# Kernel tuning notes

Measured on AMD Instinct MI355X. Metric: run time of the kernel, lower is better.

## Reference

```python
import jax, jax.numpy as jnp
import numpy as np

B, C = 8192, 4096

def _to_complex(r):
    # (..., 2) real/imag stack -> complex
    return jax.lax.complex(r[..., 0], r[..., 1])

def _to_real(z):
    return jnp.stack([jnp.real(z), jnp.imag(z)], axis=-1)

def setup_inputs() -> dict:
    key = jax.random.key(0)
    kx, ka, kd = jax.random.split(key, 3)
    x = jax.random.normal(kx, (B, C, 2), dtype=jnp.float32)
    # A, D ~ Normal(1.0, 0.01) per reset_parameters
    A = 1.0 + 0.01 * jax.random.normal(ka, (1, C, 2), dtype=jnp.float32)
    D = 1.0 + 0.01 * jax.random.normal(kd, (1, C, 2), dtype=jnp.float32)
    return {"x": x, "A": A, "D": D}

def reference(x, A, D):
    # Elementwise scale (real and imag parts scaled independently, NOT complex mul)
    xs = A * x                                   # (B, C, 2)
    # torch.fft(x, 1): complex FFT over the signal dim (channels, dim 1)
    f = jnp.fft.fft(_to_complex(xs), axis=1)     # (B, C) complex64
    fs = D * _to_real(f)                         # elementwise scale in real/imag repr
    # torch.ifft is normalized by 1/N, same as jnp.fft.ifft
    out = jnp.fft.ifft(_to_complex(fs), axis=1)  # (B, C) complex64
    return _to_real(out)                         # (B, C, 2)
```

## Files before the change

kernel.cpp:

```cpp
#include <hip/hip_runtime.h>

#define FFT_N   4096
#define THREADS 256

__device__ __forceinline__ float2 cmul(float2 a, float2 b) {
    return make_float2(a.x*b.x - a.y*b.y, a.x*b.y + a.y*b.x);
}
__device__ __forceinline__ float2 cadd(float2 a, float2 b){ return make_float2(a.x+b.x, a.y+b.y); }
__device__ __forceinline__ float2 csub(float2 a, float2 b){ return make_float2(a.x-b.x, a.y-b.y); }

template<int S>
__device__ __forceinline__ float2 muli(float2 z) {
    return (S < 0) ? make_float2(z.y, -z.x) : make_float2(-z.y, z.x);
}

template<int S>
__device__ __forceinline__ void dft4(float2 a0, float2 a1, float2 a2, float2 a3,
                                     float2& y0, float2& y1, float2& y2, float2& y3) {
    float2 e0 = cadd(a0, a2), e1 = cadd(a1, a3);
    float2 o0 = csub(a0, a2), o1 = muli<S>(csub(a1, a3));
    y0 = cadd(e0, e1); y2 = csub(e0, e1);
    y1 = cadd(o0, o1); y3 = csub(o0, o1);
}

template<int S>
__device__ __forceinline__ void dft16(float2* a) {
    const float C1 = 0.92387953251128674f;
    const float S1 = 0.38268343236508978f;
    const float R2 = 0.70710678118654752f;
    const float sg = (S < 0) ? -1.0f : 1.0f;
    const float2 w1 = make_float2( C1,  sg*S1);
    const float2 w2 = make_float2( R2,  sg*R2);
    const float2 w3 = make_float2( S1,  sg*C1);
    const float2 w6 = make_float2(-R2,  sg*R2);
    const float2 w9 = make_float2(-C1, -sg*S1);
    float2 t[16];
    dft4<S>(a[0], a[4], a[8],  a[12], t[0],  t[1],  t[2],  t[3]);
    dft4<S>(a[1], a[5], a[9],  a[13], t[4],  t[5],  t[6],  t[7]);
    dft4<S>(a[2], a[6], a[10], a[14], t[8],  t[9],  t[10], t[11]);
    dft4<S>(a[3], a[7], a[11], a[15], t[12], t[13], t[14], t[15]);
    t[5]  = cmul(t[5],  w1);  t[6]  = cmul(t[6],  w2);  t[7]  = cmul(t[7],  w3);
    t[9]  = cmul(t[9],  w2);  t[10] = muli<S>(t[10]);   t[11] = cmul(t[11], w6);
    t[13] = cmul(t[13], w3);  t[14] = cmul(t[14], w6);  t[15] = cmul(t[15], w9);
    dft4<S>(t[0], t[4], t[8],  t[12], a[0], a[4], a[8],  a[12]);
    dft4<S>(t[1], t[5], t[9],  t[13], a[1], a[5], a[9],  a[13]);
    dft4<S>(t[2], t[6], t[10], t[14], a[2], a[6], a[10], a[14]);
    dft4<S>(t[3], t[7], t[11], t[15], a[3], a[7], a[11], a[15]);
}

template<int S>
__device__ __forceinline__ void twiddle_apply(float2* R, int p, float invM) {
    float ang = 6.283185307179586f * (float)p * invM;
    if (S < 0) ang = -ang;
    float s, c;
    __sincosf(ang, &s, &c);
    float2 w[16];
    w[1] = make_float2(c, s);
    w[2] = cmul(w[1], w[1]);
    w[3] = cmul(w[2], w[1]);
    w[4] = cmul(w[2], w[2]);
    #pragma unroll
    for (int k = 5; k < 16; ++k) w[k] = cmul(w[k-4], w[4]);
    #pragma unroll
    for (int k = 1; k < 16; ++k) R[k] = cmul(R[k], w[k]);
}

__device__ __forceinline__ int swz(int i) { return i ^ (((i >> 4) & 7) << 1); }

__global__ __launch_bounds__(THREADS, 5) void afdf_fft_kernel(
    const float* __restrict__ x,
    const float* __restrict__ A,
    const float* __restrict__ D,
    float* __restrict__ out)
{
    __shared__ __align__(16) float2 sh[FFT_N];

    const int t = threadIdx.x;
    const size_t rb = (size_t)blockIdx.x * FFT_N;
    const float2* __restrict__ xr = (const float2*)x + rb;
    const float2* __restrict__ Ac = (const float2*)A;
    const float2* __restrict__ Dc = (const float2*)D;
    float2* __restrict__ o        = (float2*)out + rb;

    float2 r[16];

    {
        const int p = t;
        const int pa = p ^ (((p >> 4) & 7) << 1);
        #pragma unroll
        for (int n1 = 0; n1 < 16; ++n1) {
            float2 v = xr[p + 256*n1];
            float2 a = Ac[p + 256*n1];
            r[n1] = make_float2(a.x*v.x, a.y*v.y);
        }
        dft16<-1>(r);
        twiddle_apply<-1>(r, p, 1.0f/4096.0f);
        #pragma unroll
        for (int k = 0; k < 16; ++k) sh[pa + 256*k] = r[k];
    }
    __syncthreads();

    {
        const int b = t >> 4, p2 = t & 15, base = b*256;
        #pragma unroll
        for (int n1 = 0; n1 < 16; ++n1) r[n1] = sh[swz(base + p2 + 16*n1)];
        dft16<-1>(r);
        twiddle_apply<-1>(r, p2, 1.0f/256.0f);
        #pragma unroll
        for (int k = 0; k < 16; ++k) sh[swz(base + p2 + 16*k)] = r[k];
    }
    __syncthreads();

    {
        const int cb = 16*t;
        const int u  = (t & 7) << 1;
        #pragma unroll
        for (int m = 0; m < 8; ++m) {
            float4 v = *reinterpret_cast<const float4*>(&sh[cb + ((2*m) ^ u)]);
            r[2*m]   = make_float2(v.x, v.y);
            r[2*m+1] = make_float2(v.z, v.w);
        }
        dft16<-1>(r);
        const int k1 = t >> 4, k2 = t & 15;
        #pragma unroll
        for (int k3 = 0; k3 < 16; ++k3) {
            float2 d = Dc[256*k3 + 16*k2 + k1];
            r[k3] = make_float2(d.x*r[k3].x, d.y*r[k3].y);
        }
        dft16<+1>(r);
        #pragma unroll
        for (int m = 0; m < 8; ++m) {
            float4 v = make_float4(r[2*m].x, r[2*m].y, r[2*m+1].x, r[2*m+1].y);
            *reinterpret_cast<float4*>(&sh[cb + ((2*m) ^ u)]) = v;
        }
    }
    __syncthreads();

    {
        const int b = t >> 4, p2 = t & 15, base = b*256;
        #pragma unroll
        for (int k = 0; k < 16; ++k) r[k] = sh[swz(base + p2 + 16*k)];
        twiddle_apply<+1>(r, p2, 1.0f/256.0f);
        dft16<+1>(r);
        #pragma unroll
        for (int n1 = 0; n1 < 16; ++n1) sh[swz(base + p2 + 16*n1)] = r[n1];
    }
    __syncthreads();

    {
        const int p = t;
        const int pa = p ^ (((p >> 4) & 7) << 1);
        #pragma unroll
        for (int k = 0; k < 16; ++k) r[k] = sh[pa + 256*k];
        twiddle_apply<+1>(r, p, 1.0f/4096.0f);
        dft16<+1>(r);
        const float inv = 1.0f / 4096.0f;
        #pragma unroll
        for (int n1 = 0; n1 < 16; ++n1)
            o[p + 256*n1] = make_float2(r[n1].x*inv, r[n1].y*inv);
    }
}

extern "C" void kernel_launch(void* const* d_in, const int* in_sizes, int n_in,
                              void* d_out, int out_size, void* d_ws, size_t ws_size,
                              hipStream_t stream) {
    (void)in_sizes; (void)n_in; (void)out_size; (void)d_ws; (void)ws_size;
    const float* x = (const float*)d_in[0];
    const float* A = (const float*)d_in[1];
    const float* D = (const float*)d_in[2];
    float* out = (float*)d_out;

    afdf_fft_kernel<<<dim3(8192), dim3(THREADS), 0, stream>>>(x, A, D, out);
}
```

Before: 504.3 us.

## Process two FFT rows per block with interleaved float4 shared memory

Each block now transforms two rows at once, storing both rows' complex values interleaved as float4 in shared memory so every shared access is 16 bytes wide. The per-thread twiddle factors are computed once and reused for both rows, A and D loads are shared between the rows, and the 1/N normalisation is folded into the D scaling. This amortises twiddle computation, barriers and parameter loads per row. In exchange the grid is halved, shared memory per block doubles to 64KB, and register pressure roughly doubles (launch bounds lowered to 2), which reduces occupancy and the latency hiding that comes from it.

Measured after the change: 471.6 us. 6.5% less time.

```diff
diff --git a/kernel.cpp b/kernel.cpp
--- a/kernel.cpp
+++ b/kernel.cpp
@@ -49,7 +49,7 @@
 }
 
 template<int S>
-__device__ __forceinline__ void twiddle_apply(float2* R, int p, float invM) {
+__device__ __forceinline__ void twiddle_apply2(float2* R0, float2* R1, int p, float invM) {
     float ang = 6.283185307179586f * (float)p * invM;
     if (S < 0) ang = -ang;
     float s, c;
@@ -62,102 +62,129 @@
     #pragma unroll
     for (int k = 5; k < 16; ++k) w[k] = cmul(w[k-4], w[4]);
     #pragma unroll
-    for (int k = 1; k < 16; ++k) R[k] = cmul(R[k], w[k]);
-}
-
-__device__ __forceinline__ int swz(int i) { return i ^ (((i >> 4) & 7) << 1); }
-
-__global__ __launch_bounds__(THREADS, 5) void afdf_fft_kernel(
+    for (int k = 1; k < 16; ++k) {
+        R0[k] = cmul(R0[k], w[k]);
+        R1[k] = cmul(R1[k], w[k]);
+    }
+}
+
+__device__ __forceinline__ int swz16(int i) { return i ^ ((i >> 4) & 7); }
+
+__global__ __launch_bounds__(THREADS, 2) void afdf_fft_kernel(
     const float* __restrict__ x,
     const float* __restrict__ A,
     const float* __restrict__ D,
     float* __restrict__ out)
 {
-    __shared__ __align__(16) float2 sh[FFT_N];
+    __shared__ __align__(16) float4 sh[FFT_N];
 
     const int t = threadIdx.x;
-    const size_t rb = (size_t)blockIdx.x * FFT_N;
-    const float2* __restrict__ xr = (const float2*)x + rb;
-    const float2* __restrict__ Ac = (const float2*)A;
-    const float2* __restrict__ Dc = (const float2*)D;
-    float2* __restrict__ o        = (float2*)out + rb;
-
-    float2 r[16];
+    const size_t rb = (size_t)blockIdx.x * 2 * FFT_N;
+    const float2* __restrict__ xr0 = (const float2*)x + rb;
+    const float2* __restrict__ xr1 = xr0 + FFT_N;
+    const float2* __restrict__ Ac  = (const float2*)A;
+    const float2* __restrict__ Dc  = (const float2*)D;
+    float2* __restrict__ o0        = (float2*)out + rb;
+    float2* __restrict__ o1        = o0 + FFT_N;
+
+    float2 r0[16], r1[16];
 
     {
         const int p = t;
-        const int pa = p ^ (((p >> 4) & 7) << 1);
-        #pragma unroll
-        for (int n1 = 0; n1 < 16; ++n1) {
-            float2 v = xr[p + 256*n1];
-            float2 a = Ac[p + 256*n1];
-            r[n1] = make_float2(a.x*v.x, a.y*v.y);
-        }
-        dft16<-1>(r);
-        twiddle_apply<-1>(r, p, 1.0f/4096.0f);
-        #pragma unroll
-        for (int k = 0; k < 16; ++k) sh[pa + 256*k] = r[k];
+        #pragma unroll
+        for (int n = 0; n < 16; ++n) {
+            float2 a  = Ac[p + 256*n];
+            float2 v0 = xr0[p + 256*n];
+            float2 v1 = xr1[p + 256*n];
+            r0[n] = make_float2(a.x*v0.x, a.y*v0.y);
+            r1[n] = make_float2(a.x*v1.x, a.y*v1.y);
+        }
+        dft16<-1>(r0);
+        dft16<-1>(r1);
+        twiddle_apply2<-1>(r0, r1, p, 1.0f/4096.0f);
+        #pragma unroll
+        for (int k = 0; k < 16; ++k)
+            sh[swz16(p + 256*k)] = make_float4(r0[k].x, r0[k].y, r1[k].x, r1[k].y);
     }
     __syncthreads();
 
     {
         const int b = t >> 4, p2 = t & 15, base = b*256;
         #pragma unroll
-        for (int n1 = 0; n1 < 16; ++n1) r[n1] = sh[swz(base + p2 + 16*n1)];
-        dft16<-1>(r);
-        twiddle_apply<-1>(r, p2, 1.0f/256.0f);
-        #pragma unroll
-        for (int k = 0; k < 16; ++k) sh[swz(base + p2 + 16*k)] = r[k];
-    }
-    __syncthreads();
-
-    {
-        const int cb = 16*t;
-        const int u  = (t & 7) << 1;
-        #pragma unroll
-        for (int m = 0; m < 8; ++m) {
-            float4 v = *reinterpret_cast<const float4*>(&sh[cb + ((2*m) ^ u)]);
-            r[2*m]   = make_float2(v.x, v.y);
-            r[2*m+1] = make_float2(v.z, v.w);
-        }
-        dft16<-1>(r);
+        for (int n = 0; n < 16; ++n) {
+            float4 v = sh[swz16(base + p2 + 16*n)];
+            r0[n] = make_float2(v.x, v.y);
+            r1[n] = make_float2(v.z, v.w);
+        }
+        dft16<-1>(r0);
+        dft16<-1>(r1);
+        twiddle_apply2<-1>(r0, r1, p2, 1.0f/256.0f);
+        #pragma unroll
+        for (int k = 0; k < 16; ++k)
+            sh[swz16(base + p2 + 16*k)] = make_float4(r0[k].x, r0[k].y, r1[k].x, r1[k].y);
+    }
+    __syncthreads();
+
+    {
+        const int base = 16*t;
+        #pragma unroll
+        for (int n = 0; n < 16; ++n) {
+            float4 v = sh[swz16(base + n)];
+            r0[n] = make_float2(v.x, v.y);
+            r1[n] = make_float2(v.z, v.w);
+        }
+        dft16<-1>(r0);
+        dft16<-1>(r1);
         const int k1 = t >> 4, k2 = t & 15;
+        const float inv = 1.0f / 4096.0f;
         #pragma unroll
         for (int k3 = 0; k3 < 16; ++k3) {
             float2 d = Dc[256*k3 + 16*k2 + k1];
-            r[k3] = make_float2(d.x*r[k3].x, d.y*r[k3].y);
-        }
-        dft16<+1>(r);
-        #pragma unroll
-        for (int m = 0; m < 8; ++m) {
-            float4 v = make_float4(r[2*m].x, r[2*m].y, r[2*m+1].x, r[2*m+1].y);
-            *reinterpret_cast<float4*>(&sh[cb + ((2*m) ^ u)]) = v;
-        }
+            float dx = d.x * inv, dy = d.y * inv;
+            r0[k3] = make_float2(dx*r0[k3].x, dy*r0[k3].y);
+            r1[k3] = make_float2(dx*r1[k3].x, dy*r1[k3].y);
+        }
+        dft16<+1>(r0);
+        dft16<+1>(r1);
+        #pragma unroll
+        for (int n = 0; n < 16; ++n)
+            sh[swz16(base + n)] = make_float4(r0[n].x, r0[n].y, r1[n].x, r1[n].y);
     }
     __syncthreads();
 
     {
         const int b = t >> 4, p2 = t & 15, base = b*256;
         #pragma unroll
-        for (int k = 0; k < 16; ++k) r[k] = sh[swz(base + p2 + 16*k)];
-        twiddle_apply<+1>(r, p2, 1.0f/256.0f);
-        dft16<+1>(r);
-        #pragma unroll
-        for (int n1 = 0; n1 < 16; ++n1) sh[swz(base + p2 + 16*n1)] = r[n1];
+        for (int k = 0; k < 16; ++k) {
+            float4 v = sh[swz16(base + p2 + 16*k)];
+            r0[k] = make_float2(v.x, v.y);
+            r1[k] = make_float2(v.z, v.w);
+        }
+        twiddle_apply2<+1>(r0, r1, p2, 1.0f/256.0f);
+        dft16<+1>(r0);
+        dft16<+1>(r1);
+        #pragma unroll
+        for (int n = 0; n < 16; ++n)
+            sh[swz16(base + p2 + 16*n)] = make_float4(r0[n].x, r0[n].y, r1[n].x, r1[n].y);
     }
     __syncthreads();
 
     {
         const int p = t;
-        const int pa = p ^ (((p >> 4) & 7) << 1);
-        #pragma unroll
-        for (int k = 0; k < 16; ++k) r[k] = sh[pa + 256*k];
-        twiddle_apply<+1>(r, p, 1.0f/4096.0f);
-        dft16<+1>(r);
-        const float inv = 1.0f / 4096.0f;
-        #pragma unroll
-        for (int n1 = 0; n1 < 16; ++n1)
-            o[p + 256*n1] = make_float2(r[n1].x*inv, r[n1].y*inv);
+        #pragma unroll
+        for (int k = 0; k < 16; ++k) {
+            float4 v = sh[swz16(p + 256*k)];
+            r0[k] = make_float2(v.x, v.y);
+            r1[k] = make_float2(v.z, v.w);
+        }
+        twiddle_apply2<+1>(r0, r1, p, 1.0f/4096.0f);
+        dft16<+1>(r0);
+        dft16<+1>(r1);
+        #pragma unroll
+        for (int n1 = 0; n1 < 16; ++n1) {
+            o0[p + 256*n1] = r0[n1];
+            o1[p + 256*n1] = r1[n1];
+        }
     }
 }
 
@@ -170,5 +197,5 @@
     const float* D = (const float*)d_in[2];
     float* out = (float*)d_out;
 
-    afdf_fft_kernel<<<dim3(8192), dim3(THREADS), 0, stream>>>(x, A, D, out);
-}
+    afdf_fft_kernel<<<dim3(4096), dim3(THREADS), 0, stream>>>(x, A, D, out);
+}
```
